# Optimization experiments

Measured on AMD Instinct MI355X. Metric: run time of the kernel, lower is better.

Reference implementation:

```python
import jax, jax.numpy as jnp
import numpy as np

NUM_BANDS = 24
HID = 128
B = 8
T = 800
L = 192000


def _hann(K):
    # torch.hann_window default is periodic
    n = np.arange(K)
    return 0.5 * (1.0 - np.cos(2.0 * np.pi * n / K))


def _make_filter_bank(num_bands=NUM_BANDS, K=31):
    half = K // 2
    d = (np.arange(K) - half).astype(np.float64)
    ds = np.where(d == 0, 1.0, d)
    win = _hann(K)
    W = np.zeros((num_bands, 1, K), np.float64)
    for i in range(num_bands):
        cf = 100.0 + i * 7000.0 / num_bands
        w = np.where(d == 0, 1.0, np.sin(2.0 * np.pi * cf * ds / 24000.0) / (np.pi * ds + 1e-8))
        w = w * win
        w = w / (np.abs(w).sum() + 1e-8)
        W[i, 0] = w
    return jnp.asarray(W, jnp.float32)


def _make_noise_type_filters(K=63):
    half = K // 2
    d = (np.arange(K) - half).astype(np.float64)
    ds = np.where(d == 0, 1.0, d)
    win = _hann(K)
    f0 = np.where(d == 0, 1.0, -0.85 * np.sin(np.pi * ds / K) / (np.pi * ds + 1e-8))
    f1 = np.where(d == 0, 1.0, np.sin(np.pi * ds / (K / 2)) / (np.pi * ds + 1e-8) * np.exp(-np.abs(ds) / 5.0))
    f2 = np.sin(np.pi * d / (K * 2)) / np.maximum(1.0, np.pi * d)
    f3 = np.sin(np.pi * d / (K / 4)) / np.maximum(1.0, np.pi * d) * np.exp(-np.abs(d) / 10.0)
    F = np.stack([f0, f1, f2, f3], 0)
    F = F * win[None, :]
    F = F / (np.abs(F).sum(axis=1, keepdims=True) + 1e-8)
    return jnp.asarray(F[:, None, :], jnp.float32)  # [4,1,K]


def conv1d(x, w, pad):
    # x: [B,Cin,L], w: [Cout,Cin,K]; cross-correlation like torch Conv1d
    return jax.lax.conv_general_dilated(x, w, (1,), [(pad, pad)],
                                        dimension_numbers=('NCH', 'OIH', 'NCH'))


def linterp(x, L_out):
    # F.interpolate(mode='linear', align_corners=False) over last axis
    T_in = x.shape[-1]
    pos = (jnp.arange(L_out, dtype=x.dtype) + 0.5) * (T_in / L_out) - 0.5
    pos = jnp.clip(pos, 0.0, T_in - 1)
    i0 = jnp.floor(pos).astype(jnp.int32)
    i1 = jnp.minimum(i0 + 1, T_in - 1)
    w = pos - i0
    return jnp.take(x, i0, axis=-1) * (1.0 - w) + jnp.take(x, i1, axis=-1) * w


def _noise_gate(intensity, attack_rate):
    # intensity, attack_rate: [B,L]; audio_length > 4 always here
    diff = jnp.pad(intensity[:, 1:] - intensity[:, :-1], ((0, 0), (1, 0)))
    attack_mask = (diff > 0.1).astype(intensity.dtype)
    enhanced = jnp.clip(intensity + attack_mask * attack_rate * 0.3, 0.0, 1.0)
    inc = (diff > 0).astype(intensity.dtype)
    gate = intensity * (1.0 - inc) + enhanced * inc
    g = jnp.pad(gate, ((0, 0), (2, 2)), mode='reflect')[:, None, :]
    k = jnp.ones((1, 1, 5), gate.dtype) / 5.0
    return conv1d(g, k, 0)[:, 0, :]


def setup_inputs() -> dict:
    key = jax.random.key(0)
    ks = jax.random.split(key, 8)
    s = 0.05
    inp = {
        'condition': jax.random.normal(ks[0], (B, HID, T), jnp.float32),
        'white_noise': jax.random.normal(ks[1], (B, 1, L), jnp.float32),
        'np_w1': jax.random.normal(ks[2], (256, HID, 3), jnp.float32) * s,
        'np_b1': jnp.zeros((256,), jnp.float32),
        'np_w2': jax.random.normal(ks[3], (256, 256, 3), jnp.float32) * s,
        'np_b2': jnp.zeros((256,), jnp.float32),
        'np_w3': jax.random.normal(ks[4], (NUM_BANDS + 3, 256, 1), jnp.float32) * s,
        'np_b3': jnp.zeros((NUM_BANDS + 3,), jnp.float32),
        'ss_w1': jax.random.normal(ks[5], (128, HID, 3), jnp.float32) * s,
        'ss_b1': jnp.zeros((128,), jnp.float32),
        'ss_w2': jax.random.normal(ks[6], (4, 128, 1), jnp.float32) * s,
        'ss_b2': jnp.zeros((4,), jnp.float32),
        'fb_w': _make_filter_bank(),
        'nt_w': _make_noise_type_filters(),
        'audio_length': L,
    }
    return inp


def reference(condition, white_noise, np_w1, np_b1, np_w2, np_b2, np_w3, np_b3,
              ss_w1, ss_b1, ss_w2, ss_b2, fb_w, nt_w, audio_length):
    # noise predictor
    h = jax.nn.leaky_relu(conv1d(condition, np_w1, 1) + np_b1[None, :, None], 0.1)
    h = jax.nn.leaky_relu(conv1d(h, np_w2, 1) + np_b2[None, :, None], 0.1)
    noise_params = conv1d(h, np_w3, 0) + np_b3[None, :, None]  # [B,27,T]
    band_amps = jax.nn.sigmoid(noise_params[:, :NUM_BANDS])
    attack = jax.nn.sigmoid(noise_params[:, -3]) * 10.0
    release = jax.nn.sigmoid(noise_params[:, -2]) * 5.0  # computed but unused (as in source)
    intensity = jax.nn.sigmoid(noise_params[:, -1])
    # spectral shaper
    g = jax.nn.leaky_relu(conv1d(condition, ss_w1, 1) + ss_b1[None, :, None], 0.1)
    ntw = jax.nn.softmax(conv1d(g, ss_w2, 0) + ss_b2[None, :, None], axis=1)  # [B,4,T]
    # upsample frame-rate controls to sample rate
    band_up = linterp(band_amps, audio_length)   # [B,24,L]
    ntw_up = linterp(ntw, audio_length)          # [B,4,L]
    inten_up = linterp(intensity, audio_length)  # [B,L]
    attack_up = linterp(attack, audio_length)
    _release_up = linterp(release, audio_length)
    # noise-type filter bank (4 filters stacked as one conv)
    ftypes = conv1d(white_noise, nt_w, 31)                       # [B,4,L]
    filtered = jnp.sum(ftypes * ntw_up, axis=1, keepdims=True)   # [B,1,L]
    # 24-band filter bank stacked as one conv
    bands = conv1d(filtered, fb_w, 15)                           # [B,24,L]
    shaped = jnp.sum(bands * band_up, axis=1)                    # [B,L]
    gate = _noise_gate(inten_up, attack_up)
    return shaped * gate, gate
```

## Files before the change

### kernel.cpp

```cpp
#include <hip/hip_runtime.h>
#include <math.h>

static constexpr int B  = 8;
static constexpr int T  = 800;
static constexpr int L  = 192000;
static constexpr int NB = 24;
static constexpr float SCALE = 800.0f / 192000.0f;

typedef __bf16 bf8 __attribute__((ext_vector_type(8)));
typedef float  f4  __attribute__((ext_vector_type(4)));

__device__ __forceinline__ float sigf(float x) { return 1.0f / (1.0f + __expf(-x)); }
__device__ __forceinline__ float leaky(float x) { return x >= 0.0f ? x : 0.1f * x; }
__device__ __forceinline__ unsigned short f2bf(float f) {
    unsigned u = __float_as_uint(f);
    u = u + 0x7FFFu + ((u >> 16) & 1u);
    return (unsigned short)(u >> 16);
}
__device__ __forceinline__ float bflo(unsigned u) { return __uint_as_float(u << 16); }
__device__ __forceinline__ float bfhi(unsigned u) { return __uint_as_float(u & 0xffff0000u); }

__device__ __forceinline__ void interp_idx(int l, int& i0, int& i1, float& w) {
    float pos = ((float)l + 0.5f) * SCALE - 0.5f;
    pos = fminf(fmaxf(pos, 0.0f), (float)(T - 1));
    i0 = (int)pos;
    i1 = min(i0 + 1, T - 1);
    w = pos - (float)i0;
}

__global__ __launch_bounds__(256) void k_twm(const float* __restrict__ w1,
                                             const float* __restrict__ w2,
                                             const float* __restrict__ wss,
                                             unsigned short* __restrict__ wT1,
                                             unsigned short* __restrict__ wT2,
                                             unsigned short* __restrict__ wTs) {
    int idx = blockIdx.x * 256 + threadIdx.x;
    if (idx < 98304) {
        int tap = idx / (256 * 128), r = idx % (256 * 128);
        int cout = r / 128, cin = r % 128;
        wT1[idx] = f2bf(w1[(cout * 128 + cin) * 3 + tap]);
    } else if (idx < 98304 + 196608) {
        int j = idx - 98304;
        int tap = j / (256 * 256), r = j % (256 * 256);
        int cout = r / 256, cin = r % 256;
        wT2[j] = f2bf(w2[(cout * 256 + cin) * 3 + tap]);
    } else if (idx < 98304 + 196608 + 49152) {
        int j = idx - 294912;
        int tap = j / (128 * 128), r = j % (128 * 128);
        int cout = r / 128, cin = r % 128;
        wTs[j] = f2bf(wss[(cout * 128 + cin) * 3 + tap]);
    }
}

union SMem {
    struct {
        unsigned short xs[20 * 136];
        unsigned short h1s[18 * 264];
        unsigned short h2s[16 * 264];
        float bnd[16][25];
    } np;
    struct {
        unsigned short xs[18 * 136];
        unsigned short gs[16 * 136];
        float sv[16][5];
        float nws[16][5];
    } ss;
};

__global__ __launch_bounds__(512) void k_mega(const float* __restrict__ cond,
                                              const unsigned short* __restrict__ wT1,
                                              const float* __restrict__ b1,
                                              const unsigned short* __restrict__ wT2,
                                              const float* __restrict__ b2np,
                                              const float* __restrict__ w3,
                                              const float* __restrict__ b3,
                                              const float* __restrict__ fbw,
                                              const unsigned short* __restrict__ wTs,
                                              const float* __restrict__ bss,
                                              const float* __restrict__ w2ss,
                                              const float* __restrict__ b2ss,
                                              const float* __restrict__ ntf,
                                              float* __restrict__ h_all,
                                              float* __restrict__ g_all,
                                              float* __restrict__ attack,
                                              float* __restrict__ inten) {
    __shared__ SMem sm;
    const int b = blockIdx.y;
    const int t0 = blockIdx.x * 16;
    const int tid = threadIdx.x;
    const int wave = tid >> 6, lane = tid & 63;
    const int nfr = lane & 15;
    const int ko8 = (lane >> 4) * 8;
    const int rb = (lane >> 4) * 4;
    const int tcol = lane & 15;

    if (blockIdx.z == 0) {
        for (int i = tid; i < 20 * 128; i += 512) {
            int cin = i / 20, j = i % 20;
            int t = t0 - 2 + j;
            sm.np.xs[j * 136 + cin] = (t >= 0 && t < T) ? f2bf(cond[(b * 128 + cin) * T + t])
                                                        : (unsigned short)0;
        }
        __syncthreads();
        const int coutb = wave * 32;
        f4 a1[2][2] = {};
#pragma unroll
        for (int tap = 0; tap < 3; ++tap) {
#pragma unroll
            for (int kc = 0; kc < 128; kc += 32) {
                bf8 bv0 = *reinterpret_cast<const bf8*>(&sm.np.xs[(nfr + tap) * 136 + kc + ko8]);
                bf8 bv1 = *reinterpret_cast<const bf8*>(&sm.np.xs[(nfr + 16 + tap) * 136 + kc + ko8]);
#pragma unroll
                for (int m = 0; m < 2; ++m) {
                    bf8 av = *reinterpret_cast<const bf8*>(
                        wT1 + ((tap * 256 + coutb + m * 16 + nfr) * 128 + kc + ko8));
                    a1[0][m] = __builtin_amdgcn_mfma_f32_16x16x32_bf16(av, bv0, a1[0][m], 0, 0, 0);
                    a1[1][m] = __builtin_amdgcn_mfma_f32_16x16x32_bf16(av, bv1, a1[1][m], 0, 0, 0);
                }
            }
        }
#pragma unroll
        for (int nt = 0; nt < 2; ++nt) {
            int lcol = nt * 16 + tcol;
            if (lcol < 18) {
                int gcol = t0 - 1 + lcol;
                bool ok = (gcol >= 0 && gcol < T);
#pragma unroll
                for (int m = 0; m < 2; ++m) {
                    ushort4 pk;
                    if (ok) {
                        pk.x = f2bf(leaky(a1[nt][m][0] + b1[coutb + m * 16 + rb + 0]));
                        pk.y = f2bf(leaky(a1[nt][m][1] + b1[coutb + m * 16 + rb + 1]));
                        pk.z = f2bf(leaky(a1[nt][m][2] + b1[coutb + m * 16 + rb + 2]));
                        pk.w = f2bf(leaky(a1[nt][m][3] + b1[coutb + m * 16 + rb + 3]));
                    } else {
                        pk.x = pk.y = pk.z = pk.w = 0;
                    }
                    *reinterpret_cast<ushort4*>(&sm.np.h1s[lcol * 264 + coutb + m * 16 + rb]) = pk;
                }
            }
        }
        __syncthreads();
        f4 a2[2] = {};
#pragma unroll
        for (int tap = 0; tap < 3; ++tap) {
#pragma unroll
            for (int kc = 0; kc < 256; kc += 32) {
                bf8 bv = *reinterpret_cast<const bf8*>(&sm.np.h1s[(nfr + tap) * 264 + kc + ko8]);
#pragma unroll
                for (int m = 0; m < 2; ++m) {
                    bf8 av = *reinterpret_cast<const bf8*>(
                        wT2 + ((tap * 256 + coutb + m * 16 + nfr) * 256 + kc + ko8));
                    a2[m] = __builtin_amdgcn_mfma_f32_16x16x32_bf16(av, bv, a2[m], 0, 0, 0);
                }
            }
        }
#pragma unroll
        for (int m = 0; m < 2; ++m) {
            ushort4 pk;
            pk.x = f2bf(leaky(a2[m][0] + b2np[coutb + m * 16 + rb + 0]));
            pk.y = f2bf(leaky(a2[m][1] + b2np[coutb + m * 16 + rb + 1]));
            pk.z = f2bf(leaky(a2[m][2] + b2np[coutb + m * 16 + rb + 2]));
            pk.w = f2bf(leaky(a2[m][3] + b2np[coutb + m * 16 + rb + 3]));
            *reinterpret_cast<ushort4*>(&sm.np.h2s[tcol * 264 + coutb + m * 16 + rb]) = pk;
        }
        __syncthreads();
        for (int i = tid; i < 27 * 16; i += 512) {
            int c = i >> 4, t = i & 15;
            float s = b3[c];
            const unsigned short* hp = &sm.np.h2s[t * 264];
            const float* wp3 = w3 + c * 256;
#pragma unroll 4
            for (int kk = 0; kk < 256; kk += 8) {
                uint4 u = *reinterpret_cast<const uint4*>(hp + kk);
                float4 wa = *reinterpret_cast<const float4*>(wp3 + kk);
                float4 wb = *reinterpret_cast<const float4*>(wp3 + kk + 4);
                s += bflo(u.x) * wa.x + bfhi(u.x) * wa.y
                   + bflo(u.y) * wa.z + bfhi(u.y) * wa.w
                   + bflo(u.z) * wb.x + bfhi(u.z) * wb.y
                   + bflo(u.w) * wb.z + bfhi(u.w) * wb.w;
            }
            if (c < 24) sm.np.bnd[t][c] = sigf(s);
            else if (c == 24) attack[b * T + t0 + t] = sigf(s) * 10.0f;
            else if (c == 26) inten[b * T + t0 + t] = sigf(s);
        }
        __syncthreads();
        for (int i = tid; i < 31 * 16; i += 512) {
            int k = i >> 4, t = i & 15;
            float s = 0.0f;
#pragma unroll
            for (int c = 0; c < NB; ++c) s += sm.np.bnd[t][c] * fbw[c * 31 + k];
            h_all[(b * 31 + k) * T + t0 + t] = s;
        }
    } else {
        for (int i = tid; i < 18 * 128; i += 512) {
            int cin = i / 18, tr = i % 18;
            int t = t0 + tr - 1;
            sm.ss.xs[tr * 136 + cin] = (t >= 0 && t < T) ? f2bf(cond[(b * 128 + cin) * T + t])
                                                         : (unsigned short)0;
        }
        __syncthreads();
        const int coutb = wave * 16;
        f4 acc = {};
#pragma unroll
        for (int tap = 0; tap < 3; ++tap) {
#pragma unroll
            for (int kc = 0; kc < 128; kc += 32) {
                bf8 bv = *reinterpret_cast<const bf8*>(&sm.ss.xs[(nfr + tap) * 136 + kc + ko8]);
                bf8 av = *reinterpret_cast<const bf8*>(
                    wTs + ((tap * 128 + coutb + nfr) * 128 + kc + ko8));
                acc = __builtin_amdgcn_mfma_f32_16x16x32_bf16(av, bv, acc, 0, 0, 0);
            }
        }
        {
            ushort4 pk;
            pk.x = f2bf(leaky(acc[0] + bss[coutb + rb + 0]));
            pk.y = f2bf(leaky(acc[1] + bss[coutb + rb + 1]));
            pk.z = f2bf(leaky(acc[2] + bss[coutb + rb + 2]));
            pk.w = f2bf(leaky(acc[3] + bss[coutb + rb + 3]));
            *reinterpret_cast<ushort4*>(&sm.ss.gs[tcol * 136 + coutb + rb]) = pk;
        }
        __syncthreads();
        if (tid < 64) {
            int c = tid & 3, tl = tid >> 2;
            float s = b2ss[c];
#pragma unroll
            for (int kk = 0; kk < 128; kk += 8) {
                uint4 u = *reinterpret_cast<const uint4*>(&sm.ss.gs[tl * 136 + kk]);
                float4 wa = *reinterpret_cast<const float4*>(&w2ss[c * 128 + kk]);
                float4 wb = *reinterpret_cast<const float4*>(&w2ss[c * 128 + kk + 4]);
                s += bflo(u.x) * wa.x + bfhi(u.x) * wa.y
                   + bflo(u.y) * wa.z + bfhi(u.y) * wa.w
                   + bflo(u.z) * wb.x + bfhi(u.z) * wb.y
                   + bflo(u.w) * wb.z + bfhi(u.w) * wb.w;
            }
            sm.ss.sv[tl][c] = s;
        }
        __syncthreads();
        if (tid < 16) {
            float a0 = sm.ss.sv[tid][0], a1v = sm.ss.sv[tid][1];
            float a2v = sm.ss.sv[tid][2], a3v = sm.ss.sv[tid][3];
            float m = fmaxf(fmaxf(a0, a1v), fmaxf(a2v, a3v));
            float e0 = __expf(a0 - m), e1 = __expf(a1v - m);
            float e2 = __expf(a2v - m), e3 = __expf(a3v - m);
            float inv = 1.0f / (e0 + e1 + e2 + e3);
            sm.ss.nws[tid][0] = e0 * inv; sm.ss.nws[tid][1] = e1 * inv;
            sm.ss.nws[tid][2] = e2 * inv; sm.ss.nws[tid][3] = e3 * inv;
        }
        __syncthreads();
        for (int i = tid; i < 63 * 16; i += 512) {
            int k = i >> 4, t = i & 15;
            float s = sm.ss.nws[t][0] * ntf[k] + sm.ss.nws[t][1] * ntf[63 + k]
                    + sm.ss.nws[t][2] * ntf[126 + k] + sm.ss.nws[t][3] * ntf[189 + k];
            g_all[(b * 63 + k) * T + t0 + t] = s;
        }
    }
}

__device__ __forceinline__ float interp_T(const float* __restrict__ a, int b, int p) {
    int i0, i1; float w;
    interp_idx(p, i0, i1, w);
    return a[b * T + i0] * (1.0f - w) + a[b * T + i1] * w;
}

__device__ __forceinline__ int refl(int p) {
    return p < 0 ? -p : (p >= L ? 2 * L - 2 - p : p);
}

__global__ __launch_bounds__(256) void k_sr(const float* __restrict__ wn,
                                            const float* __restrict__ g_all,
                                            const float* __restrict__ h_all,
                                            const float* __restrict__ attack,
                                            const float* __restrict__ inten,
                                            float* __restrict__ out) {
    __shared__ float wns[348];
    __shared__ float gl[4][63];
    __shared__ float hl[4][31];
    __shared__ float flt[286];
    __shared__ float ipl[261];
    __shared__ float gp[260];
    const int b = blockIdx.y;
    const int l0 = blockIdx.x * 256;
    const int tid = threadIdx.x;
    for (int i = tid; i < 348; i += 256) {
        int p = l0 - 46 + i;
        wns[i] = (p >= 0 && p < L) ? wn[b * L + p] : 0.0f;
    }
    int fg0, fgu; float wgu;
    interp_idx(l0 - 15, fg0, fgu, wgu);
    for (int i = tid; i < 376; i += 256) {
        if (i < 252) {
            int j = i / 63, k = i % 63;
            int f = min(fg0 + j, T - 1);
            gl[j][k] = g_all[(b * 63 + k) * T + f];
        } else {
            int j2 = (i - 252) / 31, k2 = (i - 252) % 31;
            int f = min(fg0 + j2, T - 1);
            hl[j2][k2] = h_all[(b * 31 + k2) * T + f];
        }
    }
    for (int i = tid; i < 261; i += 256)
        ipl[i] = interp_T(inten, b, l0 - 3 + i);
    __syncthreads();
    for (int i = tid; i < 260; i += 256) {
        int p = l0 - 2 + i;
        int pr = refl(p);
        float cur = ipl[pr - l0 + 3];
        float prev = (pr == 0) ? cur : ipl[pr - 1 - l0 + 3];
        float diff = cur - prev;
        float ar = interp_T(attack, b, pr);
        float enh = fminf(fmaxf(cur + (diff > 0.1f ? ar * 0.3f : 0.0f), 0.0f), 1.0f);
        gp[i] = (diff > 0.0f) ? enh : cur;
    }
    for (int i = tid; i < 286; i += 256) {
        int p = l0 - 15 + i;
        float v = 0.0f;
        if (p >= 0 && p < L) {
            int i0, i1; float w;
            interp_idx(p, i0, i1, w);
            int d0 = min(max(i0 - fg0, 0), 3);
            int d1 = min(max(i1 - fg0, 0), 3);
            float a0 = 0.0f, a1 = 0.0f;
#pragma unroll
            for (int k = 0; k < 63; ++k) {
                float xk = wns[i + k];
                a0 += xk * gl[d0][k];
                a1 += xk * gl[d1][k];
            }
            v = (1.0f - w) * a0 + w * a1;
        }
        flt[i] = v;
    }
    __syncthreads();
    const int l = l0 + tid;
    int i0, i1; float w;
    interp_idx(l, i0, i1, w);
    int d0 = min(max(i0 - fg0, 0), 3);
    int d1 = min(max(i1 - fg0, 0), 3);
    float a0 = 0.0f, a1 = 0.0f;
#pragma unroll
    for (int k = 0; k < 31; ++k) {
        float xk = flt[tid + k];
        a0 += xk * hl[d0][k];
        a1 += xk * hl[d1][k];
    }
    float shaped = (1.0f - w) * a0 + w * a1;
    float g5 = (gp[tid] + gp[tid + 1] + gp[tid + 2] + gp[tid + 3] + gp[tid + 4]) * 0.2f;
    out[b * L + l] = shaped * g5;
    out[B * L + b * L + l] = g5;
}

extern "C" void kernel_launch(void* const* d_in, const int* in_sizes, int n_in,
                              void* d_out, int out_size, void* d_ws, size_t ws_size,
                              hipStream_t stream) {
    const float* cond  = (const float*)d_in[0];
    const float* wn    = (const float*)d_in[1];
    const float* np_w1 = (const float*)d_in[2];
    const float* np_b1 = (const float*)d_in[3];
    const float* np_w2 = (const float*)d_in[4];
    const float* np_b2 = (const float*)d_in[5];
    const float* np_w3 = (const float*)d_in[6];
    const float* np_b3 = (const float*)d_in[7];
    const float* ss_w1 = (const float*)d_in[8];
    const float* ss_b1 = (const float*)d_in[9];
    const float* ss_w2 = (const float*)d_in[10];
    const float* ss_b2 = (const float*)d_in[11];
    const float* fb_w  = (const float*)d_in[12];
    const float* nt_w  = (const float*)d_in[13];

    char* p = (char*)d_ws;
    unsigned short* wT1 = (unsigned short*)p; p += 196608;
    unsigned short* wT2 = (unsigned short*)p; p += 393216;
    unsigned short* wTs = (unsigned short*)p; p += 98304;
    float* attack = (float*)p; p += 25600;
    float* inten  = (float*)p; p += 25600;
    float* g_all  = (float*)p; p += 1612800;
    float* h_all  = (float*)p; p += 793600;
    float* out = (float*)d_out;

    k_twm<<<1344, 256, 0, stream>>>(np_w1, np_w2, ss_w1, wT1, wT2, wTs);
    k_mega<<<dim3(50, 8, 2), 512, 0, stream>>>(cond, wT1, np_b1, wT2, np_b2, np_w3, np_b3,
                                               fb_w, wTs, ss_b1, ss_w2, ss_b2, nt_w,
                                               h_all, g_all, attack, inten);
    k_sr<<<dim3(750, 8), 256, 0, stream>>>(wn, g_all, h_all, attack, inten, out);
}
```

Before: 168.5 us.

## Double frame tile per block in k_mega and preload weight fragments per tap

The conditioning-network kernel now processes 32 frames per block instead of 16, halving the grid. The MFMA loops preload each tap's bf16 weight fragments into registers and reuse them across the extra time tiles, so each weight load from global memory feeds twice as many frames. The cost is more registers and shared memory per block and only 400 blocks, which leaves fewer than two blocks per CU and may lower occupancy and latency hiding. Halo overhead per frame drops.

New measurement: 159.0 us. 1.06x faster.

```diff
diff --git a/kernel.cpp b/kernel.cpp
--- a/kernel.cpp
+++ b/kernel.cpp
@@ -54,16 +54,16 @@
 
 union SMem {
     struct {
-        unsigned short xs[20 * 136];
-        unsigned short h1s[18 * 264];
-        unsigned short h2s[16 * 264];
-        float bnd[16][25];
+        unsigned short xs[50 * 136];
+        unsigned short h1s[34 * 264];
+        unsigned short h2s[32 * 264];
+        float bnd[32][25];
     } np;
     struct {
-        unsigned short xs[18 * 136];
-        unsigned short gs[16 * 136];
-        float sv[16][5];
-        float nws[16][5];
+        unsigned short xs[34 * 136];
+        unsigned short gs[32 * 136];
+        float sv[32][5];
+        float nws[32][5];
     } ss;
 };
 
@@ -86,7 +86,7 @@
                                               float* __restrict__ inten) {
     __shared__ SMem sm;
     const int b = blockIdx.y;
-    const int t0 = blockIdx.x * 16;
+    const int t0 = blockIdx.x * 32;
     const int tid = threadIdx.x;
     const int wave = tid >> 6, lane = tid & 63;
     const int nfr = lane & 15;
@@ -95,34 +95,41 @@
     const int tcol = lane & 15;
 
     if (blockIdx.z == 0) {
-        for (int i = tid; i < 20 * 128; i += 512) {
-            int cin = i / 20, j = i % 20;
+        for (int i = tid; i < 50 * 128; i += 512) {
+            int cin = i / 50, j = i % 50;
             int t = t0 - 2 + j;
             sm.np.xs[j * 136 + cin] = (t >= 0 && t < T) ? f2bf(cond[(b * 128 + cin) * T + t])
                                                         : (unsigned short)0;
         }
         __syncthreads();
         const int coutb = wave * 32;
-        f4 a1[2][2] = {};
+        f4 a1[3][2] = {};
 #pragma unroll
         for (int tap = 0; tap < 3; ++tap) {
-#pragma unroll
-            for (int kc = 0; kc < 128; kc += 32) {
-                bf8 bv0 = *reinterpret_cast<const bf8*>(&sm.np.xs[(nfr + tap) * 136 + kc + ko8]);
-                bf8 bv1 = *reinterpret_cast<const bf8*>(&sm.np.xs[(nfr + 16 + tap) * 136 + kc + ko8]);
+            bf8 aw[2][4];
+#pragma unroll
+            for (int m = 0; m < 2; ++m)
+#pragma unroll
+                for (int q = 0; q < 4; ++q)
+                    aw[m][q] = *reinterpret_cast<const bf8*>(
+                        wT1 + ((tap * 256 + coutb + m * 16 + nfr) * 128 + q * 32 + ko8));
+#pragma unroll
+            for (int q = 0; q < 4; ++q) {
+                bf8 bv0 = *reinterpret_cast<const bf8*>(&sm.np.xs[(nfr + tap) * 136 + q * 32 + ko8]);
+                bf8 bv1 = *reinterpret_cast<const bf8*>(&sm.np.xs[(nfr + 16 + tap) * 136 + q * 32 + ko8]);
+                bf8 bv2 = *reinterpret_cast<const bf8*>(&sm.np.xs[(nfr + 32 + tap) * 136 + q * 32 + ko8]);
 #pragma unroll
                 for (int m = 0; m < 2; ++m) {
-                    bf8 av = *reinterpret_cast<const bf8*>(
-                        wT1 + ((tap * 256 + coutb + m * 16 + nfr) * 128 + kc + ko8));
-                    a1[0][m] = __builtin_amdgcn_mfma_f32_16x16x32_bf16(av, bv0, a1[0][m], 0, 0, 0);
-                    a1[1][m] = __builtin_amdgcn_mfma_f32_16x16x32_bf16(av, bv1, a1[1][m], 0, 0, 0);
+                    a1[0][m] = __builtin_amdgcn_mfma_f32_16x16x32_bf16(aw[m][q], bv0, a1[0][m], 0, 0, 0);
+                    a1[1][m] = __builtin_amdgcn_mfma_f32_16x16x32_bf16(aw[m][q], bv1, a1[1][m], 0, 0, 0);
+                    a1[2][m] = __builtin_amdgcn_mfma_f32_16x16x32_bf16(aw[m][q], bv2, a1[2][m], 0, 0, 0);
                 }
             }
         }
 #pragma unroll
-        for (int nt = 0; nt < 2; ++nt) {
+        for (int nt = 0; nt < 3; ++nt) {
             int lcol = nt * 16 + tcol;
-            if (lcol < 18) {
+            if (lcol < 34) {
                 int gcol = t0 - 1 + lcol;
                 bool ok = (gcol >= 0 && gcol < T);
 #pragma unroll
@@ -141,32 +148,41 @@
             }
         }
         __syncthreads();
-        f4 a2[2] = {};
+        f4 a2[2][2] = {};
 #pragma unroll
         for (int tap = 0; tap < 3; ++tap) {
-#pragma unroll
-            for (int kc = 0; kc < 256; kc += 32) {
-                bf8 bv = *reinterpret_cast<const bf8*>(&sm.np.h1s[(nfr + tap) * 264 + kc + ko8]);
+            bf8 aw[2][8];
+#pragma unroll
+            for (int m = 0; m < 2; ++m)
+#pragma unroll
+                for (int q = 0; q < 8; ++q)
+                    aw[m][q] = *reinterpret_cast<const bf8*>(
+                        wT2 + ((tap * 256 + coutb + m * 16 + nfr) * 256 + q * 32 + ko8));
+#pragma unroll
+            for (int q = 0; q < 8; ++q) {
+                bf8 bv0 = *reinterpret_cast<const bf8*>(&sm.np.h1s[(nfr + tap) * 264 + q * 32 + ko8]);
+                bf8 bv1 = *reinterpret_cast<const bf8*>(&sm.np.h1s[(nfr + 16 + tap) * 264 + q * 32 + ko8]);
 #pragma unroll
                 for (int m = 0; m < 2; ++m) {
-                    bf8 av = *reinterpret_cast<const bf8*>(
-                        wT2 + ((tap * 256 + coutb + m * 16 + nfr) * 256 + kc + ko8));
-                    a2[m] = __builtin_amdgcn_mfma_f32_16x16x32_bf16(av, bv, a2[m], 0, 0, 0);
+                    a2[0][m] = __builtin_amdgcn_mfma_f32_16x16x32_bf16(aw[m][q], bv0, a2[0][m], 0, 0, 0);
+                    a2[1][m] = __builtin_amdgcn_mfma_f32_16x16x32_bf16(aw[m][q], bv1, a2[1][m], 0, 0, 0);
                 }
             }
         }
 #pragma unroll
-        for (int m = 0; m < 2; ++m) {
-            ushort4 pk;
-            pk.x = f2bf(leaky(a2[m][0] + b2np[coutb + m * 16 + rb + 0]));
-            pk.y = f2bf(leaky(a2[m][1] + b2np[coutb + m * 16 + rb + 1]));
-            pk.z = f2bf(leaky(a2[m][2] + b2np[coutb + m * 16 + rb + 2]));
-            pk.w = f2bf(leaky(a2[m][3] + b2np[coutb + m * 16 + rb + 3]));
-            *reinterpret_cast<ushort4*>(&sm.np.h2s[tcol * 264 + coutb + m * 16 + rb]) = pk;
-        }
-        __syncthreads();
-        for (int i = tid; i < 27 * 16; i += 512) {
-            int c = i >> 4, t = i & 15;
+        for (int nv = 0; nv < 2; ++nv)
+#pragma unroll
+            for (int m = 0; m < 2; ++m) {
+                ushort4 pk;
+                pk.x = f2bf(leaky(a2[nv][m][0] + b2np[coutb + m * 16 + rb + 0]));
+                pk.y = f2bf(leaky(a2[nv][m][1] + b2np[coutb + m * 16 + rb + 1]));
+                pk.z = f2bf(leaky(a2[nv][m][2] + b2np[coutb + m * 16 + rb + 2]));
+                pk.w = f2bf(leaky(a2[nv][m][3] + b2np[coutb + m * 16 + rb + 3]));
+                *reinterpret_cast<ushort4*>(&sm.np.h2s[(nv * 16 + tcol) * 264 + coutb + m * 16 + rb]) = pk;
+            }
+        __syncthreads();
+        for (int i = tid; i < 27 * 32; i += 512) {
+            int c = i >> 5, t = i & 31;
             float s = b3[c];
             const unsigned short* hp = &sm.np.h2s[t * 264];
             const float* wp3 = w3 + c * 256;
@@ -185,43 +201,49 @@
             else if (c == 26) inten[b * T + t0 + t] = sigf(s);
         }
         __syncthreads();
-        for (int i = tid; i < 31 * 16; i += 512) {
-            int k = i >> 4, t = i & 15;
+        for (int i = tid; i < 31 * 32; i += 512) {
+            int k = i >> 5, t = i & 31;
             float s = 0.0f;
 #pragma unroll
             for (int c = 0; c < NB; ++c) s += sm.np.bnd[t][c] * fbw[c * 31 + k];
             h_all[(b * 31 + k) * T + t0 + t] = s;
         }
     } else {
-        for (int i = tid; i < 18 * 128; i += 512) {
-            int cin = i / 18, tr = i % 18;
+        for (int i = tid; i < 34 * 128; i += 512) {
+            int cin = i / 34, tr = i % 34;
             int t = t0 + tr - 1;
             sm.ss.xs[tr * 136 + cin] = (t >= 0 && t < T) ? f2bf(cond[(b * 128 + cin) * T + t])
                                                          : (unsigned short)0;
         }
         __syncthreads();
         const int coutb = wave * 16;
-        f4 acc = {};
+        f4 acc[2] = {};
 #pragma unroll
         for (int tap = 0; tap < 3; ++tap) {
-#pragma unroll
-            for (int kc = 0; kc < 128; kc += 32) {
-                bf8 bv = *reinterpret_cast<const bf8*>(&sm.ss.xs[(nfr + tap) * 136 + kc + ko8]);
-                bf8 av = *reinterpret_cast<const bf8*>(
-                    wTs + ((tap * 128 + coutb + nfr) * 128 + kc + ko8));
-                acc = __builtin_amdgcn_mfma_f32_16x16x32_bf16(av, bv, acc, 0, 0, 0);
-            }
-        }
-        {
+            bf8 aw[4];
+#pragma unroll
+            for (int q = 0; q < 4; ++q)
+                aw[q] = *reinterpret_cast<const bf8*>(
+                    wTs + ((tap * 128 + coutb + nfr) * 128 + q * 32 + ko8));
+#pragma unroll
+            for (int q = 0; q < 4; ++q) {
+                bf8 bv0 = *reinterpret_cast<const bf8*>(&sm.ss.xs[(nfr + tap) * 136 + q * 32 + ko8]);
+                bf8 bv1 = *reinterpret_cast<const bf8*>(&sm.ss.xs[(nfr + 16 + tap) * 136 + q * 32 + ko8]);
+                acc[0] = __builtin_amdgcn_mfma_f32_16x16x32_bf16(aw[q], bv0, acc[0], 0, 0, 0);
+                acc[1] = __builtin_amdgcn_mfma_f32_16x16x32_bf16(aw[q], bv1, acc[1], 0, 0, 0);
+            }
+        }
+#pragma unroll
+        for (int nv = 0; nv < 2; ++nv) {
             ushort4 pk;
-            pk.x = f2bf(leaky(acc[0] + bss[coutb + rb + 0]));
-            pk.y = f2bf(leaky(acc[1] + bss[coutb + rb + 1]));
-            pk.z = f2bf(leaky(acc[2] + bss[coutb + rb + 2]));
-            pk.w = f2bf(leaky(acc[3] + bss[coutb + rb + 3]));
-            *reinterpret_cast<ushort4*>(&sm.ss.gs[tcol * 136 + coutb + rb]) = pk;
-        }
-        __syncthreads();
-        if (tid < 64) {
+            pk.x = f2bf(leaky(acc[nv][0] + bss[coutb + rb + 0]));
+            pk.y = f2bf(leaky(acc[nv][1] + bss[coutb + rb + 1]));
+            pk.z = f2bf(leaky(acc[nv][2] + bss[coutb + rb + 2]));
+            pk.w = f2bf(leaky(acc[nv][3] + bss[coutb + rb + 3]));
+            *reinterpret_cast<ushort4*>(&sm.ss.gs[(nv * 16 + tcol) * 136 + coutb + rb]) = pk;
+        }
+        __syncthreads();
+        if (tid < 128) {
             int c = tid & 3, tl = tid >> 2;
             float s = b2ss[c];
 #pragma unroll
@@ -237,7 +259,7 @@
             sm.ss.sv[tl][c] = s;
         }
         __syncthreads();
-        if (tid < 16) {
+        if (tid < 32) {
             float a0 = sm.ss.sv[tid][0], a1v = sm.ss.sv[tid][1];
             float a2v = sm.ss.sv[tid][2], a3v = sm.ss.sv[tid][3];
             float m = fmaxf(fmaxf(a0, a1v), fmaxf(a2v, a3v));
@@ -248,8 +270,8 @@
             sm.ss.nws[tid][2] = e2 * inv; sm.ss.nws[tid][3] = e3 * inv;
         }
         __syncthreads();
-        for (int i = tid; i < 63 * 16; i += 512) {
-            int k = i >> 4, t = i & 15;
+        for (int i = tid; i < 63 * 32; i += 512) {
+            int k = i >> 5, t = i & 31;
             float s = sm.ss.nws[t][0] * ntf[k] + sm.ss.nws[t][1] * ntf[63 + k]
                     + sm.ss.nws[t][2] * ntf[126 + k] + sm.ss.nws[t][3] * ntf[189 + k];
             g_all[(b * 63 + k) * T + t0 + t] = s;
@@ -379,7 +401,7 @@
     float* out = (float*)d_out;
 
     k_twm<<<1344, 256, 0, stream>>>(np_w1, np_w2, ss_w1, wT1, wT2, wTs);
-    k_mega<<<dim3(50, 8, 2), 512, 0, stream>>>(cond, wT1, np_b1, wT2, np_b2, np_w3, np_b3,
+    k_mega<<<dim3(25, 8, 2), 512, 0, stream>>>(cond, wT1, np_b1, wT2, np_b2, np_w3, np_b3,
                                                fb_w, wTs, ss_b1, ss_w2, ss_b2, nt_w,
                                                h_all, g_all, attack, inten);
     k_sr<<<dim3(750, 8), 256, 0, stream>>>(wn, g_all, h_all, attack, inten, out);
```
